# Performance work log

Measured on AMD Instinct MI355X. Metric: run time of the kernel, lower is better.

## Reference

```python
import jax, jax.numpy as jnp
import numpy as np

RES = 128
SH_DIM = 9            # (deg+1)^2, deg=2
CH = SH_DIM * 3 + 1   # 28: 3*9 SH rgb coeffs + 1 sigma
AABB_MIN = -1.0
AABB_MAX = 1.0
STEP = (AABB_MAX - AABB_MIN) / (RES - 1)   # voxel_len = mean(aabb_size/(res-1))
UNIFORM = 0.5
N_SAMPLES = int(RES * 3 / UNIFORM)         # plenoxels count: 768
EPS = 1e-10


def sh_encode_deg2(d):
    # real spherical harmonics basis, degree 2 (9 coefficients), on normalized dirs
    d = d / jnp.linalg.norm(d, axis=-1, keepdims=True)
    x, y, z = d[..., 0], d[..., 1], d[..., 2]
    C0 = 0.28209479177387814
    C1 = 0.4886025119029199
    C20, C21, C22 = 1.0925484305920792, -1.0925484305920792, 0.31539156525252005
    C23, C24 = -1.0925484305920792, 0.5462742152960396
    return jnp.stack([
        jnp.full_like(x, C0),
        -C1 * y, C1 * z, -C1 * x,
        C20 * x * y, C21 * y * z, C22 * (2.0 * z * z - x * x - y * y),
        C23 * x * z, C24 * (x * x - y * y),
    ], axis=-1)


def grid_sample_3d(grid, pts):
    # grid: [D,H,W,C]; pts: [...,3] in [-1,1], (x,y,z) with x->W, y->H, z->D.
    # Matches torch F.grid_sample(mode='bilinear', padding_mode='zeros', align_corners=True).
    D, H, W, C = grid.shape
    lead = pts.shape[:-1]
    p = pts.reshape(-1, 3)
    x = (p[:, 0] + 1.0) * 0.5 * (W - 1)
    y = (p[:, 1] + 1.0) * 0.5 * (H - 1)
    z = (p[:, 2] + 1.0) * 0.5 * (D - 1)
    x0f, y0f, z0f = jnp.floor(x), jnp.floor(y), jnp.floor(z)
    fx, fy, fz = x - x0f, y - y0f, z - z0f
    x0 = x0f.astype(jnp.int32)
    y0 = y0f.astype(jnp.int32)
    z0 = z0f.astype(jnp.int32)
    flat = grid.reshape(-1, C)
    out = jnp.zeros((p.shape[0], C), grid.dtype)
    for dz in (0, 1):
        for dy in (0, 1):
            for dx in (0, 1):
                xi, yi, zi = x0 + dx, y0 + dy, z0 + dz
                valid = (xi >= 0) & (xi < W) & (yi >= 0) & (yi < H) & (zi >= 0) & (zi < D)
                w = ((fx if dx else 1.0 - fx)
                     * (fy if dy else 1.0 - fy)
                     * (fz if dz else 1.0 - fz)) * valid
                idx = (jnp.clip(zi, 0, D - 1) * H + jnp.clip(yi, 0, H - 1)) * W + jnp.clip(xi, 0, W - 1)
                out = out + w[:, None] * flat[idx]
    return out.reshape(lead + (C,))


def setup_inputs() -> dict:
    key = jax.random.key(0)
    k1, k2, k3 = jax.random.split(key, 3)
    B = 4096
    # origins on a radius-3 sphere, aimed at jittered targets inside the unit box
    o = jax.random.normal(k1, (B, 3), dtype=jnp.float32)
    rays_o = 3.0 * o / jnp.linalg.norm(o, axis=-1, keepdims=True)
    tgt = jax.random.uniform(k2, (B, 3), dtype=jnp.float32, minval=-0.5, maxval=0.5)
    d = tgt - rays_o
    rays_d = d / jnp.linalg.norm(d, axis=-1, keepdims=True)
    grid_data = 0.1 * jax.random.normal(k3, (RES ** 3, CH), dtype=jnp.float32)
    grid_data = grid_data.at[:, -1].add(0.1)  # ini_sigma offset
    return {"rays_d": rays_d, "rays_o": rays_o, "grid_data": grid_data}


def reference(rays_d, rays_o, grid_data):
    B = rays_d.shape[0]
    aabb_lo = jnp.full((3,), AABB_MIN, rays_o.dtype)
    aabb_hi = jnp.full((3,), AABB_MAX, rays_o.dtype)
    # ray-AABB intersection (no_grad in torch)
    t_pos = (aabb_hi - rays_o) / rays_d
    t_neg = (aabb_lo - rays_o) / rays_d
    t_in = jnp.minimum(t_pos, t_neg)
    t_out = jnp.maximum(t_pos, t_neg)
    start = jnp.max(t_in, axis=-1)                  # [B]
    stop = jnp.min(t_out, axis=-1, keepdims=True)   # [B,1]
    # tensor_linspace from start+u*step to start+u*step*n, then clamp max=stop
    w = jnp.linspace(0.0, 1.0, N_SAMPLES, dtype=rays_o.dtype)  # [S]
    s0 = start + UNIFORM * STEP
    s1 = start + UNIFORM * STEP * N_SAMPLES
    intersections = s0[:, None] * (1.0 - w) + s1[:, None] * w   # [B,S]
    intersections = jnp.minimum(intersections, stop)
    t = intersections[:, :-1]                                    # [B,S-1]
    pts = rays_o[:, None, :] + t[:, :, None] * rays_d[:, None, :]
    pts = (pts - AABB_MIN) * (2.0 / (AABB_MAX - AABB_MIN)) - 1.0  # normalize to [-1,1]
    # trilinear sample of the voxel grid (torch layout: D=res0,H=res1,W=res2; x->W)
    interp = grid_sample_3d(grid_data.reshape(RES, RES, RES, CH), pts)  # [B,S-1,CH]
    sigma = interp[..., -1]
    rgb_sh = interp[..., :-1].reshape(B, N_SAMPLES - 1, 3, SH_DIM)
    sh = sh_encode_deg2(rays_d)                                   # [B,9]
    rgb = jnp.einsum('bsck,bk->bsc', rgb_sh, sh)
    # volumetric rendering
    dists = jnp.diff(intersections, axis=1) * jnp.linalg.norm(rays_d, axis=-1, keepdims=True)
    alpha = 1.0 - jnp.exp(-jax.nn.relu(sigma) * dists)
    cum_light = jnp.concatenate(
        [jnp.ones((B, 1), alpha.dtype), jnp.cumprod(1.0 - alpha[:, :-1] + EPS, axis=-1)], axis=-1)
    abs_light = alpha * cum_light
    acc_map = abs_light.sum(-1)
    rgb_map = (abs_light[..., None] * jax.nn.sigmoid(rgb)).sum(-2)
    depth = (abs_light * t).sum(-1)
    rgb_map = rgb_map + (1.0 - acc_map[:, None])  # white background
    return rgb_map, alpha, depth
```

## Files before the change

kernel.cpp:

```cpp
#include <hip/hip_runtime.h>
#include <math.h>

#define RESG 128
#define CHG 28
#define NT 767
#define NLBKT 48

template <int PAT>
static __device__ __forceinline__ float swz(float x) {
    return __int_as_float(__builtin_amdgcn_ds_swizzle(__float_as_int(x), PAT));
}

__global__ __launch_bounds__(1024) void prep_sort(
    const float* __restrict__ rays_d, const float* __restrict__ rays_o,
    int* __restrict__ perm, int B)
{
    __shared__ int cnt[64];
    __shared__ int off[64];
    __shared__ unsigned char keys[4096];
    const int tid = threadIdx.x;
    if (tid < 64) cnt[tid] = 0;
    __syncthreads();
    for (int r = tid; r < B; r += 1024) {
        const float ox = rays_o[r*3+0], oy = rays_o[r*3+1], oz = rays_o[r*3+2];
        const float dx = rays_d[r*3+0], dy = rays_d[r*3+1], dz = rays_d[r*3+2];
        float txp = (1.0f - ox)/dx, txn = (-1.0f - ox)/dx;
        float typ = (1.0f - oy)/dy, tyn = (-1.0f - oy)/dy;
        float tzp = (1.0f - oz)/dz, tzn = (-1.0f - oz)/dz;
        const float start = fmaxf(fmaxf(fminf(txp,txn), fminf(typ,tyn)), fminf(tzp,tzn));
        const float stop  = fminf(fminf(fmaxf(txp,txn), fmaxf(typ,tyn)), fmaxf(tzp,tzn));
        int n_proc = (int)((stop - start) * 127.0f) + 2;
        n_proc = n_proc < 0 ? 0 : (n_proc > NT ? NT : n_proc);
        int lvl = n_proc >> 4; if (lvl > NLBKT-1) lvl = NLBKT-1;
        const int k = (NLBKT-1) - lvl;
        keys[r] = (unsigned char)k;
        atomicAdd(&cnt[k], 1);
    }
    __syncthreads();
    if (tid < 64) {
        int v = cnt[tid];
        int incl = v;
        #pragma unroll
        for (int o2 = 1; o2 < 64; o2 <<= 1) {
            const int n = __shfl_up(incl, o2, 64);
            if ((tid & 63) >= o2) incl += n;
        }
        off[tid] = incl - v;
    }
    __syncthreads();
    for (int r = tid; r < B; r += 1024) {
        const int slot = atomicAdd(&off[keys[r]], 1);
        perm[slot] = r;
    }
}

__global__ __launch_bounds__(256) void nerf_grid_kernel(
    const float* __restrict__ rays_d,
    const float* __restrict__ rays_o,
    const float* __restrict__ grid,
    const int*   __restrict__ perm,
    float* __restrict__ out_rgb,
    float* __restrict__ out_alpha,
    float* __restrict__ out_depth)
{
    const int ray  = perm[blockIdx.x];
    const int tid  = threadIdx.x;
    const int lane = tid & 63;
    const int wave = tid >> 6;

    const float EPSC   = 1e-10f;
    const float INV127 = 1.0f / 127.0f;

    __shared__ float a_lds[NT + 1];
    __shared__ float r_lds[NT + 1];
    __shared__ float g_lds[NT + 1];
    __shared__ float b_lds[NT + 1];
    __shared__ float wprod[4];
    __shared__ float red[4][5];

    const float ox = rays_o[ray*3+0], oy = rays_o[ray*3+1], oz = rays_o[ray*3+2];
    const float dx = rays_d[ray*3+0], dy = rays_d[ray*3+1], dz = rays_d[ray*3+2];
    const float dnorm = sqrtf(dx*dx + dy*dy + dz*dz);

    float txp = (1.0f - ox)/dx, txn = (-1.0f - ox)/dx;
    float typ = (1.0f - oy)/dy, tyn = (-1.0f - oy)/dy;
    float tzp = (1.0f - oz)/dz, tzn = (-1.0f - oz)/dz;
    const float start = fmaxf(fmaxf(fminf(txp,txn), fminf(typ,tyn)), fminf(tzp,tzn));
    const float stop  = fminf(fminf(fmaxf(txp,txn), fmaxf(typ,tyn)), fmaxf(tzp,tzn));

    int n_proc = (int)((stop - start) * 127.0f) + 2;
    n_proc = n_proc < 0 ? 0 : (n_proc > NT ? NT : n_proc);

    const float inv = 1.0f/dnorm;
    const float nx = dx*inv, ny = dy*inv, nz = dz*inv;
    float sh0, sh1, sh2, sh3, sh4, sh5, sh6, sh7, sh8;
    {
        const float C0 = 0.28209479177387814f;
        const float C1 = 0.4886025119029199f;
        const float C20 = 1.0925484305920792f, C21 = -1.0925484305920792f;
        const float C22 = 0.31539156525252005f;
        const float C23 = -1.0925484305920792f, C24 = 0.5462742152960396f;
        sh0 = C0;   sh1 = -C1*ny; sh2 = C1*nz; sh3 = -C1*nx;
        sh4 = C20*nx*ny; sh5 = C21*ny*nz;
        sh6 = C22*(2.0f*nz*nz - nx*nx - ny*ny);
        sh7 = C23*nx*nz; sh8 = C24*(nx*nx - ny*ny);
    }

    const int samp   = lane >> 3;
    const int corner = lane & 7;
    const int cdx = corner & 1, cdy = (corner >> 1) & 1, cdz = corner >> 2;

    for (int base = wave*8; base < n_proc; base += 32) {
        const int s = base + samp;
        float rr = 0.0f, gg = 0.0f, bb = 0.0f, sg = 0.0f;
        float t0 = 0.0f, dist = 0.0f;
        bool live = false;
        if (s < n_proc) {
            t0 = fminf(start + (float)(s+1)*INV127, stop);
            const float t1 = fminf(start + (float)(s+2)*INV127, stop);
            dist = (t1 - t0) * dnorm;
            live = dist > 0.0f;
        }
        if (live) {
            const float gx = (ox + t0*dx + 1.0f)*63.5f;
            const float gy = (oy + t0*dy + 1.0f)*63.5f;
            const float gz = (oz + t0*dz + 1.0f)*63.5f;
            const float fx0 = floorf(gx), fy0 = floorf(gy), fz0 = floorf(gz);
            const float fx = gx - fx0, fy = gy - fy0, fz = gz - fz0;
            const int xi = (int)fx0 + cdx;
            const int yi = (int)fy0 + cdy;
            const int zi = (int)fz0 + cdz;
            const bool valid = ((unsigned)xi < (unsigned)RESG) &
                               ((unsigned)yi < (unsigned)RESG) &
                               ((unsigned)zi < (unsigned)RESG);
            const float w = (cdx ? fx : 1.0f-fx) *
                            (cdy ? fy : 1.0f-fy) *
                            (cdz ? fz : 1.0f-fz);
            if (valid && w != 0.0f) {
                const float4* row = (const float4*)(grid + (size_t)(((zi*RESG) + yi)*RESG + xi)*CHG);
                const float4 v0 = row[0], v1 = row[1], v2 = row[2], v3 = row[3];
                const float4 v4 = row[4], v5 = row[5], v6 = row[6];
                rr = w*(v0.x*sh0 + v0.y*sh1 + v0.z*sh2 + v0.w*sh3 +
                        v1.x*sh4 + v1.y*sh5 + v1.z*sh6 + v1.w*sh7 + v2.x*sh8);
                gg = w*(v2.y*sh0 + v2.z*sh1 + v2.w*sh2 + v3.x*sh3 +
                        v3.y*sh4 + v3.z*sh5 + v3.w*sh6 + v4.x*sh7 + v4.y*sh8);
                bb = w*(v4.z*sh0 + v4.w*sh1 + v5.x*sh2 + v5.y*sh3 +
                        v5.z*sh4 + v5.w*sh5 + v6.x*sh6 + v6.y*sh7 + v6.z*sh8);
                sg = w*v6.w;
            }
        }
        rr += swz<0x041F>(rr); gg += swz<0x041F>(gg); bb += swz<0x041F>(bb); sg += swz<0x041F>(sg);
        rr += swz<0x081F>(rr); gg += swz<0x081F>(gg); bb += swz<0x081F>(bb); sg += swz<0x081F>(sg);
        rr += swz<0x101F>(rr); gg += swz<0x101F>(gg); bb += swz<0x101F>(bb); sg += swz<0x101F>(sg);

        if (corner == 0 && s < n_proc) {
            a_lds[s] = live ? 1.0f - expf(-fmaxf(sg, 0.0f)*dist) : 0.0f;
            r_lds[s] = 1.0f/(1.0f + expf(-rr));
            g_lds[s] = 1.0f/(1.0f + expf(-gg));
            b_lds[s] = 1.0f/(1.0f + expf(-bb));
        }
    }
    __syncthreads();

    for (int s = tid; s < NT; s += 256)
        out_alpha[(size_t)ray*NT + s] = (s < n_proc) ? a_lds[s] : 0.0f;

    float a_r[3], q_r[3], t_r[3], rr_r[3], gg_r[3], bb_r[3];
    #pragma unroll
    for (int k = 0; k < 3; ++k) {
        const int s = tid*3 + k;
        float a = 0.0f, rr = 0.0f, gg = 0.0f, bb = 0.0f, tt = 0.0f;
        if (s < NT) {
            tt = fminf(start + (float)(s+1)*INV127, stop);
            if (s < n_proc) {
                a = a_lds[s];
                rr = r_lds[s]; gg = g_lds[s]; bb = b_lds[s];
            }
        }
        a_r[k] = a; q_r[k] = (s < NT) ? (1.0f - a + EPSC) : 1.0f;
        t_r[k] = tt; rr_r[k] = rr; gg_r[k] = gg; bb_r[k] = bb;
    }

    const float P = q_r[0]*q_r[1]*q_r[2];
    float incl = P;
    #pragma unroll
    for (int off2 = 1; off2 < 64; off2 <<= 1) {
        const float n = __shfl_up(incl, off2, 64);
        if (lane >= off2) incl *= n;
    }
    float excl = __shfl_up(incl, 1, 64);
    if (lane == 0) excl = 1.0f;

    if (lane == 63) wprod[wave] = incl;
    __syncthreads();
    float wpre = 1.0f;
    for (int w2 = 0; w2 < 4; ++w2) if (w2 < wave) wpre *= wprod[w2];

    float cum = wpre * excl;
    float accA = 0.0f, accR = 0.0f, accG = 0.0f, accB = 0.0f, accD = 0.0f;
    #pragma unroll
    for (int k = 0; k < 3; ++k) {
        const float abs_l = a_r[k] * cum;
        accA += abs_l;
        accR += abs_l * rr_r[k];
        accG += abs_l * gg_r[k];
        accB += abs_l * bb_r[k];
        accD += abs_l * t_r[k];
        cum *= q_r[k];
    }

    #pragma unroll
    for (int off2 = 32; off2 > 0; off2 >>= 1) {
        accA += __shfl_down(accA, off2, 64);
        accR += __shfl_down(accR, off2, 64);
        accG += __shfl_down(accG, off2, 64);
        accB += __shfl_down(accB, off2, 64);
        accD += __shfl_down(accD, off2, 64);
    }
    if (lane == 0) {
        red[wave][0] = accA; red[wave][1] = accR; red[wave][2] = accG;
        red[wave][3] = accB; red[wave][4] = accD;
    }
    __syncthreads();
    if (tid == 0) {
        float A = 0.0f, R = 0.0f, G = 0.0f, Bv = 0.0f, D = 0.0f;
        #pragma unroll
        for (int w2 = 0; w2 < 4; ++w2) {
            A += red[w2][0]; R += red[w2][1]; G += red[w2][2];
            Bv += red[w2][3]; D += red[w2][4];
        }
        const float bg = 1.0f - A;
        out_rgb[ray*3+0] = R  + bg;
        out_rgb[ray*3+1] = G  + bg;
        out_rgb[ray*3+2] = Bv + bg;
        out_depth[ray] = D;
    }
}

extern "C" void kernel_launch(void* const* d_in, const int* in_sizes, int n_in,
                              void* d_out, int out_size, void* d_ws, size_t ws_size,
                              hipStream_t stream) {
    const float* rays_d = (const float*)d_in[0];
    const float* rays_o = (const float*)d_in[1];
    const float* grid   = (const float*)d_in[2];
    const int B = in_sizes[0] / 3;

    float* out       = (float*)d_out;
    float* out_rgb   = out;
    float* out_alpha = out + (size_t)B*3;
    float* out_depth = out + (size_t)B*3 + (size_t)B*NT;

    int* perm = (int*)d_ws;

    prep_sort<<<1, 1024, 0, stream>>>(rays_d, rays_o, perm, B);
    nerf_grid_kernel<<<B, 256, 0, stream>>>(rays_d, rays_o, grid, perm,
                                            out_rgb, out_alpha, out_depth);
}
```

Measured before the change: 83.33 us.

## Halve block size, branchless clamped gathers, bf16 LDS colors, fast exp/rcp

Shrinks each ray block from 4 to 2 waves, with each thread covering 6 samples in the scan. The trilinear gather loses its divergent branch: coordinates are clamped and invalid corners get zero weight while still issuing loads. Sigmoid colors are stored in LDS as bf16 to cut shared memory use, and exp/division are replaced by fast intrinsics. This aims to raise occupancy and remove branch divergence, at the cost of some precision and extra loads for dead samples.

```diff
diff --git a/kernel.cpp b/kernel.cpp
--- a/kernel.cpp
+++ b/kernel.cpp
@@ -9,6 +9,13 @@
 template <int PAT>
 static __device__ __forceinline__ float swz(float x) {
     return __int_as_float(__builtin_amdgcn_ds_swizzle(__float_as_int(x), PAT));
+}
+static __device__ __forceinline__ unsigned short f2bf(float x) {
+    unsigned u = __float_as_uint(x);
+    return (unsigned short)((u + 0x7FFFu + ((u >> 16) & 1u)) >> 16);
+}
+static __device__ __forceinline__ float bf2f(unsigned short h) {
+    return __uint_as_float(((unsigned)h) << 16);
 }
 
 __global__ __launch_bounds__(1024) void prep_sort(
@@ -54,7 +61,7 @@
     }
 }
 
-__global__ __launch_bounds__(256) void nerf_grid_kernel(
+__global__ __launch_bounds__(128) void nerf_grid_kernel(
     const float* __restrict__ rays_d,
     const float* __restrict__ rays_o,
     const float* __restrict__ grid,
@@ -71,12 +78,11 @@
     const float EPSC   = 1e-10f;
     const float INV127 = 1.0f / 127.0f;
 
-    __shared__ float a_lds[NT + 1];
-    __shared__ float r_lds[NT + 1];
-    __shared__ float g_lds[NT + 1];
-    __shared__ float b_lds[NT + 1];
-    __shared__ float wprod[4];
-    __shared__ float red[4][5];
+    __shared__ float        a_lds[NT + 1];
+    __shared__ unsigned int rg_lds[NT + 1];
+    __shared__ unsigned short b_lds[NT + 1];
+    __shared__ float wprod[2];
+    __shared__ float red[2][5];
 
     const float ox = rays_o[ray*3+0], oy = rays_o[ray*3+1], oz = rays_o[ray*3+2];
     const float dx = rays_d[ray*3+0], dy = rays_d[ray*3+1], dz = rays_d[ray*3+2];
@@ -109,80 +115,74 @@
     const int samp   = lane >> 3;
     const int corner = lane & 7;
     const int cdx = corner & 1, cdy = (corner >> 1) & 1, cdz = corner >> 2;
-
-    for (int base = wave*8; base < n_proc; base += 32) {
+    const char* gridc = (const char*)grid;
+
+    for (int base = wave*8; base < n_proc; base += 16) {
         const int s = base + samp;
-        float rr = 0.0f, gg = 0.0f, bb = 0.0f, sg = 0.0f;
-        float t0 = 0.0f, dist = 0.0f;
-        bool live = false;
-        if (s < n_proc) {
-            t0 = fminf(start + (float)(s+1)*INV127, stop);
-            const float t1 = fminf(start + (float)(s+2)*INV127, stop);
-            dist = (t1 - t0) * dnorm;
-            live = dist > 0.0f;
-        }
-        if (live) {
-            const float gx = (ox + t0*dx + 1.0f)*63.5f;
-            const float gy = (oy + t0*dy + 1.0f)*63.5f;
-            const float gz = (oz + t0*dz + 1.0f)*63.5f;
-            const float fx0 = floorf(gx), fy0 = floorf(gy), fz0 = floorf(gz);
-            const float fx = gx - fx0, fy = gy - fy0, fz = gz - fz0;
-            const int xi = (int)fx0 + cdx;
-            const int yi = (int)fy0 + cdy;
-            const int zi = (int)fz0 + cdz;
-            const bool valid = ((unsigned)xi < (unsigned)RESG) &
-                               ((unsigned)yi < (unsigned)RESG) &
-                               ((unsigned)zi < (unsigned)RESG);
-            const float w = (cdx ? fx : 1.0f-fx) *
-                            (cdy ? fy : 1.0f-fy) *
-                            (cdz ? fz : 1.0f-fz);
-            if (valid && w != 0.0f) {
-                const float4* row = (const float4*)(grid + (size_t)(((zi*RESG) + yi)*RESG + xi)*CHG);
-                const float4 v0 = row[0], v1 = row[1], v2 = row[2], v3 = row[3];
-                const float4 v4 = row[4], v5 = row[5], v6 = row[6];
-                rr = w*(v0.x*sh0 + v0.y*sh1 + v0.z*sh2 + v0.w*sh3 +
-                        v1.x*sh4 + v1.y*sh5 + v1.z*sh6 + v1.w*sh7 + v2.x*sh8);
-                gg = w*(v2.y*sh0 + v2.z*sh1 + v2.w*sh2 + v3.x*sh3 +
-                        v3.y*sh4 + v3.z*sh5 + v3.w*sh6 + v4.x*sh7 + v4.y*sh8);
-                bb = w*(v4.z*sh0 + v4.w*sh1 + v5.x*sh2 + v5.y*sh3 +
-                        v5.z*sh4 + v5.w*sh5 + v6.x*sh6 + v6.y*sh7 + v6.z*sh8);
-                sg = w*v6.w;
-            }
-        }
+        const float t0 = fminf(fmaf((float)(s+1), INV127, start), stop);
+        const float t1 = fminf(fmaf((float)(s+2), INV127, start), stop);
+        const float dist = (t1 - t0) * dnorm;
+        const bool live = (s < n_proc) && (dist > 0.0f);
+
+        const float gx = fminf(fmaxf((ox + t0*dx + 1.0f)*63.5f, 0.0f), 127.0f);
+        const float gy = fminf(fmaxf((oy + t0*dy + 1.0f)*63.5f, 0.0f), 127.0f);
+        const float gz = fminf(fmaxf((oz + t0*dz + 1.0f)*63.5f, 0.0f), 127.0f);
+        const float fx0 = floorf(gx), fy0 = floorf(gy), fz0 = floorf(gz);
+        const float fx = gx - fx0, fy = gy - fy0, fz = gz - fz0;
+        const int ix = (int)fx0, iy = (int)fy0, iz = (int)fz0;
+
+        const int Bv   = ((iz*RESG + iy)*RESG + ix)*112;
+        const int offx = cdx ? ((ix < RESG-1) ? 112 : 0) : 0;
+        const int offy = cdy ? ((iy < RESG-1) ? 112*RESG : 0) : 0;
+        const int offz = cdz ? ((iz < RESG-1) ? 112*RESG*RESG : 0) : 0;
+        const unsigned rowB = (unsigned)(Bv + offx + offy + offz);
+
+        const float liveF = live ? 1.0f : 0.0f;
+        const float w = (cdx ? fx : 1.0f-fx) *
+                        (cdy ? fy : 1.0f-fy) *
+                        ((cdz ? fz : 1.0f-fz) * liveF);
+
+        const float4* row = (const float4*)(gridc + (size_t)rowB);
+        const float4 v0 = row[0], v1 = row[1], v2 = row[2], v3 = row[3];
+        const float4 v4 = row[4], v5 = row[5], v6 = row[6];
+        float rr = w*(v0.x*sh0 + v0.y*sh1 + v0.z*sh2 + v0.w*sh3 +
+                      v1.x*sh4 + v1.y*sh5 + v1.z*sh6 + v1.w*sh7 + v2.x*sh8);
+        float gg = w*(v2.y*sh0 + v2.z*sh1 + v2.w*sh2 + v3.x*sh3 +
+                      v3.y*sh4 + v3.z*sh5 + v3.w*sh6 + v4.x*sh7 + v4.y*sh8);
+        float bb = w*(v4.z*sh0 + v4.w*sh1 + v5.x*sh2 + v5.y*sh3 +
+                      v5.z*sh4 + v5.w*sh5 + v6.x*sh6 + v6.y*sh7 + v6.z*sh8);
+        float sg = w*v6.w;
+
         rr += swz<0x041F>(rr); gg += swz<0x041F>(gg); bb += swz<0x041F>(bb); sg += swz<0x041F>(sg);
         rr += swz<0x081F>(rr); gg += swz<0x081F>(gg); bb += swz<0x081F>(bb); sg += swz<0x081F>(sg);
         rr += swz<0x101F>(rr); gg += swz<0x101F>(gg); bb += swz<0x101F>(bb); sg += swz<0x101F>(sg);
 
         if (corner == 0 && s < n_proc) {
-            a_lds[s] = live ? 1.0f - expf(-fmaxf(sg, 0.0f)*dist) : 0.0f;
-            r_lds[s] = 1.0f/(1.0f + expf(-rr));
-            g_lds[s] = 1.0f/(1.0f + expf(-gg));
-            b_lds[s] = 1.0f/(1.0f + expf(-bb));
-        }
-    }
-    __syncthreads();
-
-    for (int s = tid; s < NT; s += 256)
+            a_lds[s] = live ? (1.0f - __expf(-fmaxf(sg, 0.0f)*dist)) : 0.0f;
+            const float r1 = __builtin_amdgcn_rcpf(1.0f + __expf(-rr));
+            const float g1 = __builtin_amdgcn_rcpf(1.0f + __expf(-gg));
+            const float b1 = __builtin_amdgcn_rcpf(1.0f + __expf(-bb));
+            rg_lds[s] = ((unsigned)f2bf(r1) << 16) | (unsigned)f2bf(g1);
+            b_lds[s]  = f2bf(b1);
+        }
+    }
+    __syncthreads();
+
+    for (int s = tid; s < NT; s += 128)
         out_alpha[(size_t)ray*NT + s] = (s < n_proc) ? a_lds[s] : 0.0f;
 
-    float a_r[3], q_r[3], t_r[3], rr_r[3], gg_r[3], bb_r[3];
-    #pragma unroll
-    for (int k = 0; k < 3; ++k) {
-        const int s = tid*3 + k;
-        float a = 0.0f, rr = 0.0f, gg = 0.0f, bb = 0.0f, tt = 0.0f;
+    const int s0i = tid * 6;
+    float prod = 1.0f;
+    #pragma unroll
+    for (int k = 0; k < 6; ++k) {
+        const int s = s0i + k;
         if (s < NT) {
-            tt = fminf(start + (float)(s+1)*INV127, stop);
-            if (s < n_proc) {
-                a = a_lds[s];
-                rr = r_lds[s]; gg = g_lds[s]; bb = b_lds[s];
-            }
-        }
-        a_r[k] = a; q_r[k] = (s < NT) ? (1.0f - a + EPSC) : 1.0f;
-        t_r[k] = tt; rr_r[k] = rr; gg_r[k] = gg; bb_r[k] = bb;
-    }
-
-    const float P = q_r[0]*q_r[1]*q_r[2];
-    float incl = P;
+            const float a = (s < n_proc) ? a_lds[s] : 0.0f;
+            prod *= (1.0f - a + EPSC);
+        }
+    }
+
+    float incl = prod;
     #pragma unroll
     for (int off2 = 1; off2 < 64; off2 <<= 1) {
         const float n = __shfl_up(incl, off2, 64);
@@ -193,20 +193,27 @@
 
     if (lane == 63) wprod[wave] = incl;
     __syncthreads();
-    float wpre = 1.0f;
-    for (int w2 = 0; w2 < 4; ++w2) if (w2 < wave) wpre *= wprod[w2];
+    const float wpre = (wave == 1) ? wprod[0] : 1.0f;
 
     float cum = wpre * excl;
     float accA = 0.0f, accR = 0.0f, accG = 0.0f, accB = 0.0f, accD = 0.0f;
     #pragma unroll
-    for (int k = 0; k < 3; ++k) {
-        const float abs_l = a_r[k] * cum;
-        accA += abs_l;
-        accR += abs_l * rr_r[k];
-        accG += abs_l * gg_r[k];
-        accB += abs_l * bb_r[k];
-        accD += abs_l * t_r[k];
-        cum *= q_r[k];
+    for (int k = 0; k < 6; ++k) {
+        const int s = s0i + k;
+        if (s < NT) {
+            const float a = (s < n_proc) ? a_lds[s] : 0.0f;
+            const float abs_l = a * cum;
+            if (s < n_proc) {
+                const unsigned rg = rg_lds[s];
+                const float tt = fminf(fmaf((float)(s+1), INV127, start), stop);
+                accA += abs_l;
+                accR += abs_l * bf2f((unsigned short)(rg >> 16));
+                accG += abs_l * bf2f((unsigned short)(rg & 0xFFFFu));
+                accB += abs_l * bf2f(b_lds[s]);
+                accD += abs_l * tt;
+            }
+            cum *= (1.0f - a + EPSC);
+        }
     }
 
     #pragma unroll
@@ -223,12 +230,11 @@
     }
     __syncthreads();
     if (tid == 0) {
-        float A = 0.0f, R = 0.0f, G = 0.0f, Bv = 0.0f, D = 0.0f;
-        #pragma unroll
-        for (int w2 = 0; w2 < 4; ++w2) {
-            A += red[w2][0]; R += red[w2][1]; G += red[w2][2];
-            Bv += red[w2][3]; D += red[w2][4];
-        }
+        const float A  = red[0][0] + red[1][0];
+        const float R  = red[0][1] + red[1][1];
+        const float G  = red[0][2] + red[1][2];
+        const float Bv = red[0][3] + red[1][3];
+        const float D  = red[0][4] + red[1][4];
         const float bg = 1.0f - A;
         out_rgb[ray*3+0] = R  + bg;
         out_rgb[ray*3+1] = G  + bg;
@@ -253,6 +259,6 @@
     int* perm = (int*)d_ws;
 
     prep_sort<<<1, 1024, 0, stream>>>(rays_d, rays_o, perm, B);
-    nerf_grid_kernel<<<B, 256, 0, stream>>>(rays_d, rays_o, grid, perm,
+    nerf_grid_kernel<<<B, 128, 0, stream>>>(rays_d, rays_o, grid, perm,
                                             out_rgb, out_alpha, out_depth);
 }
```

After: 87.91 us. +5.5%, slower.
